# Optimization experiments

Hardware: AMD Instinct MI355X
Metric: run time of the kernel (lower is better)

Reference implementation:

```python
import jax, jax.numpy as jnp
import numpy as np

DIM = 1024
HEADS = 16
B, N = 4, 1024

def setup_inputs() -> dict:
    key = jax.random.key(0)
    k1, k2, k3 = jax.random.split(key, 3)
    x = jax.random.normal(k1, (B, N, DIM), dtype=jnp.float32)
    # xavier-uniform-ish init scale
    Wqkv = jax.random.normal(k2, (3 * DIM, DIM), dtype=jnp.float32) * (1.0 / np.sqrt(DIM))
    bqkv = jnp.zeros((3 * DIM,), dtype=jnp.float32)
    W1 = jax.random.normal(k3, (DIM, DIM), dtype=jnp.float32) * (1.0 / np.sqrt(DIM))
    b1 = jnp.zeros((DIM,), dtype=jnp.float32)
    return {"x": x, "Wqkv": Wqkv, "bqkv": bqkv, "W1": W1, "b1": b1}

def reference(x, Wqkv, bqkv, W1, b1):
    b, n, dim = x.shape
    h = HEADS
    d = dim // h
    scale = dim ** (-0.5)  # NOTE: module scales by full dim, not head dim
    qkv = x @ Wqkv.T + bqkv  # [b, n, 3*dim]
    qkv = qkv.reshape(b, n, 3, h, d)
    q = jnp.transpose(qkv[:, :, 0], (0, 2, 1, 3))  # [b, h, n, d]
    k = jnp.transpose(qkv[:, :, 1], (0, 2, 1, 3))
    v = jnp.transpose(qkv[:, :, 2], (0, 2, 1, 3))
    dots = jnp.einsum('bhid,bhjd->bhij', q, k) * scale
    attn = jax.nn.softmax(dots, axis=-1)
    out = jnp.einsum('bhij,bhjd->bhid', attn, v)
    out = jnp.transpose(out, (0, 2, 1, 3)).reshape(b, n, dim)
    out = out @ W1.T + b1
    return out
```

## Files before the change

kernel.cpp:

```cpp
#include <hip/hip_runtime.h>
#include <cmath>

typedef __bf16 bf16;
typedef __bf16 bf16x8 __attribute__((ext_vector_type(8)));
typedef __bf16 bf16x4 __attribute__((ext_vector_type(4)));
typedef float f32x4 __attribute__((ext_vector_type(4)));

#define MFMA16(a, b, c) __builtin_amdgcn_mfma_f32_16x16x32_bf16(a, b, c, 0, 0, 0)

__device__ __forceinline__ void load_lds16(const void* g, void* l) {
    __builtin_amdgcn_global_load_lds(
        (const __attribute__((address_space(1))) void*)g,
        (__attribute__((address_space(3))) void*)l, 16, 0, 0);
}

__device__ __forceinline__ bf16x8 load8(const bf16* p) { return *(const bf16x8*)p; }
__device__ __forceinline__ bf16x8 load8(const float* p) {
    float4 f0 = *(const float4*)p;
    float4 f1 = *(const float4*)(p + 4);
    bf16x8 r;
    r[0] = (bf16)f0.x; r[1] = (bf16)f0.y; r[2] = (bf16)f0.z; r[3] = (bf16)f0.w;
    r[4] = (bf16)f1.x; r[5] = (bf16)f1.y; r[6] = (bf16)f1.z; r[7] = (bf16)f1.w;
    return r;
}

__global__ __launch_bounds__(256) void cvt3(
    const float* __restrict__ s0, bf16* __restrict__ d0, int n0,
    const float* __restrict__ s1, bf16* __restrict__ d1, int n1,
    const float* __restrict__ s2, bf16* __restrict__ d2, int n2)
{
    int i = blockIdx.x * 256 + threadIdx.x;
    const float* s; bf16* d; int base;
    if (i < n0)                { s = s0; d = d0; base = i; }
    else if (i < n0 + n1)      { s = s1; d = d1; base = i - n0; }
    else if (i < n0 + n1 + n2) { s = s2; d = d2; base = i - n0 - n1; }
    else return;
    *(bf16x8*)(d + (size_t)base * 8) = load8(s + (size_t)base * 8);
}

template <int EPI, typename TB, int BN>
__global__ __launch_bounds__(256) void gemm_bt(
    const bf16* __restrict__ A, const TB* __restrict__ Bm,
    const float* __restrict__ bias,
    bf16* __restrict__ qo, bf16* __restrict__ ko, bf16* __restrict__ vto,
    float* __restrict__ C, int M, int N, int K)
{
    constexpr int WN = BN / 2;
    constexpr int JN = WN / 16;
    constexpr int SLOTS = (128 + BN) * 8;

    __shared__ bf16 As[128 * 64];
    __shared__ bf16 Bs[BN * 64];

    const int tid = threadIdx.x;
    const int l   = tid & 63;
    const int w   = tid >> 6;
    const int wm  = w & 1, wn = w >> 1;
    const int l15 = l & 15;
    const int g   = l >> 4;
    const int swz = l15 & 7;
    const int m0  = blockIdx.y * 128;
    const int n0  = blockIdx.x * BN;

    f32x4 acc[4][JN] = {};

    for (int k0 = 0; k0 < K; k0 += 64) {
        __syncthreads();
        #pragma unroll
        for (int it = 0; it < SLOTS / 256; ++it) {
            int s = it * 256 + w * 64 + l;
            if (s < 1024) {
                int row = s >> 3, pc = s & 7;
                int lc  = pc ^ (row & 7);
                load_lds16(A + (size_t)(m0 + row) * K + k0 + lc * 8, &As[s * 8]);
            } else {
                int t = s - 1024;
                int row = t >> 3, pc = t & 7;
                int lc  = pc ^ (row & 7);
                if constexpr (sizeof(TB) == 2) {
                    load_lds16(Bm + (size_t)(n0 + row) * K + k0 + lc * 8, &Bs[t * 8]);
                } else {
                    *(bf16x8*)&Bs[t * 8] = load8(Bm + (size_t)(n0 + row) * K + k0 + lc * 8);
                }
            }
        }
        __syncthreads();
        #pragma unroll
        for (int kk = 0; kk < 64; kk += 32) {
            bf16x8 aF[4], bF[JN];
            #pragma unroll
            for (int i = 0; i < 4; ++i)
                aF[i] = *(const bf16x8*)&As[(wm * 64 + i * 16 + l15) * 64
                                            + ((((kk >> 3) + g) ^ swz) * 8)];
            #pragma unroll
            for (int j = 0; j < JN; ++j)
                bF[j] = *(const bf16x8*)&Bs[(wn * WN + j * 16 + l15) * 64
                                            + ((((kk >> 3) + g) ^ swz) * 8)];
            #pragma unroll
            for (int i = 0; i < 4; ++i)
                #pragma unroll
                for (int j = 0; j < JN; ++j)
                    acc[i][j] = MFMA16(aF[i], bF[j], acc[i][j]);
        }
    }

    #pragma unroll
    for (int j = 0; j < JN; ++j) {
        int gcol = n0 + wn * WN + j * 16 + l15;
        float bv = bias[gcol];
        if (EPI == 0) {
            int which = gcol >> 10;
            int h  = (gcol >> 6) & 15;
            int dd = gcol & 63;
            if (which == 2) {
                #pragma unroll
                for (int i = 0; i < 4; ++i) {
                    int grow0 = m0 + wm * 64 + i * 16 + g * 4;
                    int b     = grow0 >> 10;
                    int npos  = grow0 & 1023;
                    size_t bh = (size_t)(b * 16 + h);
                    bf16x4 pv;
                    #pragma unroll
                    for (int r = 0; r < 4; ++r)
                        pv[r] = (bf16)(acc[i][j][r] + bv);
                    *(bf16x4*)&vto[(bh * 64 + dd) * 1024 + npos] = pv;
                }
            } else {
                #pragma unroll
                for (int i = 0; i < 4; ++i) {
                    #pragma unroll
                    for (int r = 0; r < 4; ++r) {
                        int grow = m0 + wm * 64 + i * 16 + g * 4 + r;
                        int b    = grow >> 10;
                        int npos = grow & 1023;
                        float v  = acc[i][j][r] + bv;
                        size_t bh = (size_t)(b * 16 + h);
                        if (which == 0)
                            qo[(bh * 1024 + npos) * 64 + dd] = (bf16)v;
                        else
                            ko[(bh * 1024 + npos) * 64 + dd] = (bf16)v;
                    }
                }
            }
        } else {
            #pragma unroll
            for (int i = 0; i < 4; ++i)
                #pragma unroll
                for (int r = 0; r < 4; ++r) {
                    int grow = m0 + wm * 64 + i * 16 + g * 4 + r;
                    C[(size_t)grow * N + gcol] = acc[i][j][r] + bv;
                }
        }
    }
}

__global__ __launch_bounds__(512, 4) void attn_fused(
    const bf16* __restrict__ qb, const bf16* __restrict__ kb,
    const bf16* __restrict__ vtb, bf16* __restrict__ attn)
{
    __shared__ bf16 Ks[2][64 * 64];
    __shared__ bf16 Vts[2][64 * 64];
    __shared__ bf16 Ps[8][2][16][32];

    const int tid = threadIdx.x;
    const int l   = tid & 63;
    const int w   = tid >> 6;
    const int wq  = w & 3;
    const int wh  = w >> 2;
    const int l15 = l & 15;
    const int g   = l >> 4;
    const int swz = l15 & 7;
    const int bid = blockIdx.x;
    const int bh  = bid & 63;
    const int qc  = bid >> 6;
    const int m0  = qc * 128;

    const bf16* q_bh  = qb  + (size_t)bh * 65536;
    const bf16* k_bh  = kb  + (size_t)bh * 65536;
    const bf16* vt_bh = vtb + (size_t)bh * 65536;

    bf16x8 qf[2][2];
    #pragma unroll
    for (int qg = 0; qg < 2; ++qg)
        #pragma unroll
        for (int kk = 0; kk < 2; ++kk)
            qf[qg][kk] = *(const bf16x8*)(q_bh
                + (size_t)(m0 + wq * 32 + qg * 16 + l15) * 64 + kk * 32 + g * 8);

    f32x4 o[2][4] = {};
    float lsum[2] = {0.f, 0.f};

    const float C_EXP = 0.04508422f;

    auto stage = [&](int buf, int j0) {
        int s   = tid;
        int row = s >> 3, pc = s & 7;
        int lc  = pc ^ (row & 7);
        load_lds16(k_bh + (size_t)(j0 + row) * 64 + lc * 8, &Ks[buf][s * 8]);
        load_lds16(vt_bh + (size_t)row * 1024 + j0 + lc * 8, &Vts[buf][s * 8]);
    };

    stage(0, 0);

    for (int t = 0; t < 16; ++t) {
        const int c = t & 1;
        __syncthreads();
        if (t < 15) stage(c ^ 1, (t + 1) * 64);

        f32x4 s4[2][2] = {};
        #pragma unroll
        for (int kk = 0; kk < 2; ++kk) {
            bf16x8 kf[2];
            #pragma unroll
            for (int jsl = 0; jsl < 2; ++jsl)
                kf[jsl] = *(const bf16x8*)&Ks[c][((wh * 2 + jsl) * 16 + l15) * 64
                                                 + (((kk * 4 + g) ^ swz) * 8)];
            __builtin_amdgcn_s_setprio(1);
            #pragma unroll
            for (int qg = 0; qg < 2; ++qg)
                #pragma unroll
                for (int jsl = 0; jsl < 2; ++jsl)
                    s4[qg][jsl] = MFMA16(kf[jsl], qf[qg][kk], s4[qg][jsl]);
            __builtin_amdgcn_s_setprio(0);
        }

        #pragma unroll
        for (int qg = 0; qg < 2; ++qg) {
            #pragma unroll
            for (int jsl = 0; jsl < 2; ++jsl) {
                bf16x4 pk;
                float ps = 0.f;
                #pragma unroll
                for (int r = 0; r < 4; ++r) {
                    float p = exp2f(s4[qg][jsl][r] * C_EXP);
                    ps += p;
                    pk[r] = (bf16)p;
                }
                lsum[qg] += ps;
                *(bf16x4*)&Ps[w][qg][l15][(((jsl * 2 + (g >> 1)) ^ (l15 & 3)) * 8)
                                          + (g & 1) * 4] = pk;
            }
        }

        bf16x8 vf[4];
        #pragma unroll
        for (int ns = 0; ns < 4; ++ns)
            vf[ns] = *(const bf16x8*)&Vts[c][(ns * 16 + l15) * 64
                                             + (((wh * 4 + g) ^ swz) * 8)];
        __builtin_amdgcn_s_setprio(1);
        #pragma unroll
        for (int qg = 0; qg < 2; ++qg) {
            bf16x8 pf = *(const bf16x8*)&Ps[w][qg][l15][(g ^ (l15 & 3)) * 8];
            #pragma unroll
            for (int ns = 0; ns < 4; ++ns)
                o[qg][ns] = MFMA16(pf, vf[ns], o[qg][ns]);
        }
        __builtin_amdgcn_s_setprio(0);
    }

    float tden[2];
    #pragma unroll
    for (int qg = 0; qg < 2; ++qg) {
        float t = lsum[qg];
        t += __shfl_xor(t, 16);
        t += __shfl_xor(t, 32);
        tden[qg] = t;
    }

    float* R0 = (float*)&Ks[0][0];
    float* R1 = (float*)&Vts[0][0];
    float* DN = (float*)&Ps[0][0][0][0];
    __syncthreads();
    if (wh == 1) {
        #pragma unroll
        for (int ns = 0; ns < 4; ++ns) {
            *(f32x4*)&R0[((wq * 64 + l) * 4 + ns) * 4] = o[0][ns];
            *(f32x4*)&R1[((wq * 64 + l) * 4 + ns) * 4] = o[1][ns];
        }
        DN[(wq * 2 + 0) * 64 + l] = tden[0];
        DN[(wq * 2 + 1) * 64 + l] = tden[1];
    }
    __syncthreads();
    if (wh == 0) {
        #pragma unroll
        for (int ns = 0; ns < 4; ++ns) {
            o[0][ns] += *(const f32x4*)&R0[((wq * 64 + l) * 4 + ns) * 4];
            o[1][ns] += *(const f32x4*)&R1[((wq * 64 + l) * 4 + ns) * 4];
        }
        tden[0] += DN[(wq * 2 + 0) * 64 + l];
        tden[1] += DN[(wq * 2 + 1) * 64 + l];

        #pragma unroll
        for (int qg = 0; qg < 2; ++qg) {
            #pragma unroll
            for (int r = 0; r < 4; ++r) {
                float inv = 1.0f / __shfl(tden[qg], g * 4 + r);
                int grow = m0 + wq * 32 + qg * 16 + g * 4 + r;
                size_t obase = ((size_t)(bh >> 4) * 1024 + grow) * 1024
                               + (bh & 15) * 64;
                #pragma unroll
                for (int ns = 0; ns < 4; ++ns)
                    attn[obase + ns * 16 + l15] = (bf16)(o[qg][ns][r] * inv);
            }
        }
    }
}

extern "C" void kernel_launch(void* const* d_in, const int* in_sizes, int n_in,
                              void* d_out, int out_size, void* d_ws, size_t ws_size,
                              hipStream_t stream)
{
    const float* x    = (const float*)d_in[0];
    const float* Wqkv = (const float*)d_in[1];
    const float* bqkv = (const float*)d_in[2];
    const float* W1   = (const float*)d_in[3];
    const float* b1   = (const float*)d_in[4];
    float* out = (float*)d_out;

    const size_t SEG = (size_t)4 * 16 * 1024 * 64;
    bf16* xbf  = (bf16*)d_ws;
    bf16* qb   = xbf + SEG;
    bf16* kb   = qb + SEG;
    bf16* vtb  = kb + SEG;
    bf16* attnb = xbf;
    bf16* wqkvbf = vtb + SEG;
    bf16* w1bf   = wqkvbf + 3145728;

    const bool cw = ws_size >= (size_t)(5 * SEG) * sizeof(bf16);

    const int nx = 524288;
    const int nw = cw ? 393216 : 0;
    const int n1 = cw ? 131072 : 0;
    const int tot = nx + nw + n1;
    cvt3<<<dim3((tot + 255) / 256), 256, 0, stream>>>(
        x, xbf, nx, Wqkv, wqkvbf, nw, W1, w1bf, n1);

    if (cw)
        gemm_bt<0, bf16, 128><<<dim3(24, 32), 256, 0, stream>>>(
            xbf, wqkvbf, bqkv, qb, kb, vtb, nullptr, 4096, 3072, 1024);
    else
        gemm_bt<0, float, 128><<<dim3(24, 32), 256, 0, stream>>>(
            xbf, Wqkv, bqkv, qb, kb, vtb, nullptr, 4096, 3072, 1024);

    attn_fused<<<dim3(512), 512, 0, stream>>>(qb, kb, vtb, attnb);

    if (cw)
        gemm_bt<1, bf16, 64><<<dim3(16, 32), 256, 0, stream>>>(
            attnb, w1bf, b1, nullptr, nullptr, nullptr, out, 4096, 1024, 1024);
    else
        gemm_bt<1, float, 64><<<dim3(16, 32), 256, 0, stream>>>(
            attnb, W1, b1, nullptr, nullptr, nullptr, out, 4096, 1024, 1024);
}
```

Before: 167.7 us.

## Load K and V fragments directly from global memory, dropping LDS staging

The attention kernel no longer double-buffers K and V^T tiles in shared memory. Each wave now loads its MFMA fragments straight from global memory (relying on L2/L1 reuse), which removes the per-iteration __syncthreads and the LDS round trip. The reduction scratch gets dedicated shared buffers so the final barrier before reuse can go. The cost is redundant global traffic, since each tile is reloaded by several waves, plus exposed load latency that is only partly hidden by unroll 2.

```diff
diff --git a/kernel.cpp b/kernel.cpp
--- a/kernel.cpp
+++ b/kernel.cpp
@@ -158,9 +158,10 @@
     const bf16* __restrict__ qb, const bf16* __restrict__ kb,
     const bf16* __restrict__ vtb, bf16* __restrict__ attn)
 {
-    __shared__ bf16 Ks[2][64 * 64];
-    __shared__ bf16 Vts[2][64 * 64];
     __shared__ bf16 Ps[8][2][16][32];
+    __shared__ float R0[4][64][16];
+    __shared__ float R1[4][64][16];
+    __shared__ float DNs[8][64];
 
     const int tid = threadIdx.x;
     const int l   = tid & 63;
@@ -169,7 +170,6 @@
     const int wh  = w >> 2;
     const int l15 = l & 15;
     const int g   = l >> 4;
-    const int swz = l15 & 7;
     const int bid = blockIdx.x;
     const int bh  = bid & 63;
     const int qc  = bid >> 6;
@@ -192,35 +192,33 @@
 
     const float C_EXP = 0.04508422f;
 
-    auto stage = [&](int buf, int j0) {
-        int s   = tid;
-        int row = s >> 3, pc = s & 7;
-        int lc  = pc ^ (row & 7);
-        load_lds16(k_bh + (size_t)(j0 + row) * 64 + lc * 8, &Ks[buf][s * 8]);
-        load_lds16(vt_bh + (size_t)row * 1024 + j0 + lc * 8, &Vts[buf][s * 8]);
-    };
-
-    stage(0, 0);
-
+    #pragma unroll 2
     for (int t = 0; t < 16; ++t) {
-        const int c = t & 1;
-        __syncthreads();
-        if (t < 15) stage(c ^ 1, (t + 1) * 64);
+        const int j0 = t * 64;
+
+        bf16x8 kf[2][2];
+        #pragma unroll
+        for (int kk = 0; kk < 2; ++kk)
+            #pragma unroll
+            for (int jsl = 0; jsl < 2; ++jsl)
+                kf[kk][jsl] = *(const bf16x8*)(k_bh
+                    + (size_t)(j0 + (wh * 2 + jsl) * 16 + l15) * 64
+                    + kk * 32 + g * 8);
+        bf16x8 vf[4];
+        #pragma unroll
+        for (int ns = 0; ns < 4; ++ns)
+            vf[ns] = *(const bf16x8*)(vt_bh
+                + (size_t)(ns * 16 + l15) * 1024 + j0 + (wh * 4 + g) * 8);
 
         f32x4 s4[2][2] = {};
         #pragma unroll
         for (int kk = 0; kk < 2; ++kk) {
-            bf16x8 kf[2];
-            #pragma unroll
-            for (int jsl = 0; jsl < 2; ++jsl)
-                kf[jsl] = *(const bf16x8*)&Ks[c][((wh * 2 + jsl) * 16 + l15) * 64
-                                                 + (((kk * 4 + g) ^ swz) * 8)];
             __builtin_amdgcn_s_setprio(1);
             #pragma unroll
             for (int qg = 0; qg < 2; ++qg)
                 #pragma unroll
                 for (int jsl = 0; jsl < 2; ++jsl)
-                    s4[qg][jsl] = MFMA16(kf[jsl], qf[qg][kk], s4[qg][jsl]);
+                    s4[qg][jsl] = MFMA16(kf[kk][jsl], qf[qg][kk], s4[qg][jsl]);
             __builtin_amdgcn_s_setprio(0);
         }
 
@@ -242,11 +240,6 @@
             }
         }
 
-        bf16x8 vf[4];
-        #pragma unroll
-        for (int ns = 0; ns < 4; ++ns)
-            vf[ns] = *(const bf16x8*)&Vts[c][(ns * 16 + l15) * 64
-                                             + (((wh * 4 + g) ^ swz) * 8)];
         __builtin_amdgcn_s_setprio(1);
         #pragma unroll
         for (int qg = 0; qg < 2; ++qg) {
@@ -267,28 +260,24 @@
         tden[qg] = t;
     }
 
-    float* R0 = (float*)&Ks[0][0];
-    float* R1 = (float*)&Vts[0][0];
-    float* DN = (float*)&Ps[0][0][0][0];
-    __syncthreads();
     if (wh == 1) {
         #pragma unroll
         for (int ns = 0; ns < 4; ++ns) {
-            *(f32x4*)&R0[((wq * 64 + l) * 4 + ns) * 4] = o[0][ns];
-            *(f32x4*)&R1[((wq * 64 + l) * 4 + ns) * 4] = o[1][ns];
-        }
-        DN[(wq * 2 + 0) * 64 + l] = tden[0];
-        DN[(wq * 2 + 1) * 64 + l] = tden[1];
+            *(f32x4*)&R0[wq][l][ns * 4] = o[0][ns];
+            *(f32x4*)&R1[wq][l][ns * 4] = o[1][ns];
+        }
+        DNs[wq * 2 + 0][l] = tden[0];
+        DNs[wq * 2 + 1][l] = tden[1];
     }
     __syncthreads();
     if (wh == 0) {
         #pragma unroll
         for (int ns = 0; ns < 4; ++ns) {
-            o[0][ns] += *(const f32x4*)&R0[((wq * 64 + l) * 4 + ns) * 4];
-            o[1][ns] += *(const f32x4*)&R1[((wq * 64 + l) * 4 + ns) * 4];
-        }
-        tden[0] += DN[(wq * 2 + 0) * 64 + l];
-        tden[1] += DN[(wq * 2 + 1) * 64 + l];
+            o[0][ns] += *(const f32x4*)&R0[wq][l][ns * 4];
+            o[1][ns] += *(const f32x4*)&R1[wq][l][ns * 4];
+        }
+        tden[0] += DNs[wq * 2 + 0][l];
+        tden[1] += DNs[wq * 2 + 1][l];
 
         #pragma unroll
         for (int qg = 0; qg < 2; ++qg) {
```

Measured after the change: 194.4 us. 15.9% more time.
